# Optimization experiments

Hardware: AMD Instinct MI355X
Metric: run time of the kernel (lower is better)

## Reference

```python
import jax, jax.numpy as jnp
import numpy as np

N_NODES = 100000
N_EDGES = 1600000
N_GRAPHS = 64
DIMS = [128, 128, 128, 128]
IN_CH = 4


def setup_inputs() -> dict:
    key = jax.random.key(0)
    ks = jax.random.split(key, 24)
    d = {}
    d['x'] = jax.random.normal(ks[0], (N_NODES, IN_CH), dtype=jnp.float32)
    d['metadata'] = jax.random.normal(ks[1], (N_GRAPHS, 1), dtype=jnp.float32)
    d['edge_index'] = jax.random.randint(ks[2], (2, N_EDGES), 0, N_NODES, dtype=jnp.int32)
    d['batch'] = jnp.sort(jax.random.randint(ks[3], (N_NODES,), 0, N_GRAPHS, dtype=jnp.int32))
    dims_in = [IN_CH] + DIMS[:-1]
    ki = 4
    for i, (din, dout) in enumerate(zip(dims_in, DIMS), start=1):
        s = 1.0 / np.sqrt(din)
        d[f'w_rel{i}'] = jax.random.normal(ks[ki], (din, dout), dtype=jnp.float32) * s; ki += 1
        d[f'b_rel{i}'] = jnp.zeros((dout,), dtype=jnp.float32)
        d[f'w_root{i}'] = jax.random.normal(ks[ki], (din, dout), dtype=jnp.float32) * s; ki += 1
    d['convm_w'] = jax.random.normal(ks[ki], (4,), dtype=jnp.float32); ki += 1
    d['convm_b'] = jnp.zeros((4,), dtype=jnp.float32)
    fin = DIMS[3] * 2 + 4
    d['fc_w'] = jax.random.normal(ks[ki], (fin, DIMS[3]), dtype=jnp.float32) / np.sqrt(fin); ki += 1
    d['fc_b'] = jnp.zeros((DIMS[3],), dtype=jnp.float32)
    d['fc2_w'] = jax.random.normal(ks[ki], (DIMS[3], 1), dtype=jnp.float32) / np.sqrt(DIMS[3]); ki += 1
    d['fc2_b'] = jnp.zeros((1,), dtype=jnp.float32)
    return d


def _graph_conv(x, src, dst, w_rel, b_rel, w_root):
    # PyG GraphConv (aggr='add'): out_i = lin_rel(sum_{j->i} x_j) + lin_root(x_i)
    agg = jax.ops.segment_sum(x[src], dst, num_segments=N_NODES)
    return agg @ w_rel + b_rel + x @ w_root


def reference(x, metadata, edge_index, batch,
              w_rel1, b_rel1, w_root1,
              w_rel2, b_rel2, w_root2,
              w_rel3, b_rel3, w_root3,
              w_rel4, b_rel4, w_root4,
              convm_w, convm_b, fc_w, fc_b, fc2_w, fc2_b):
    src, dst = edge_index[0], edge_index[1]
    h = jax.nn.relu(_graph_conv(x, src, dst, w_rel1, b_rel1, w_root1))
    h = jax.nn.relu(_graph_conv(h, src, dst, w_rel2, b_rel2, w_root2))
    h = jax.nn.relu(_graph_conv(h, src, dst, w_rel3, b_rel3, w_root3))
    h = jax.nn.relu(_graph_conv(h, src, dst, w_rel4, b_rel4, w_root4))
    # global pools per graph
    counts = jax.ops.segment_sum(jnp.ones((N_NODES,), h.dtype), batch, num_segments=N_GRAPHS)
    x_sum = jax.ops.segment_sum(h, batch, num_segments=N_GRAPHS)
    x_mean = x_sum / jnp.maximum(counts, 1.0)[:, None]
    x_max = jax.ops.segment_max(h, batch, num_segments=N_GRAPHS)
    x_max = jnp.where(counts[:, None] > 0, x_max, 0.0)
    # metadata branch: Conv1d(1,4,k=1) on [B,1,1] -> [B,4]
    m = jax.nn.relu(metadata * convm_w[None, :] + convm_b[None, :])  # [B,4]
    x_c = jnp.concatenate([x_max, x_mean, m], axis=1)  # [B, 2*d+4]
    out = jax.nn.relu(x_c @ fc_w + fc_b) @ fc2_w + fc2_b
    return out[:, 0]
```

## Files before the change

kernel.cpp:

```cpp
#include <hip/hip_runtime.h>

#define N_NODES 100000
#define N_EDGES 1600000
#define N_GRAPHS 64

typedef __attribute__((ext_vector_type(8))) short bf16x8;
typedef __attribute__((ext_vector_type(4))) float f32x4;

__device__ __forceinline__ unsigned int f2bf(float f) {
  unsigned int u = __float_as_uint(f);
  return (u + 0x7FFFu + ((u >> 16) & 1u)) >> 16;
}
#define BLO(u) __uint_as_float((u) << 16)
#define BHI(u) __uint_as_float((u) & 0xFFFF0000u)

__device__ __forceinline__ void split8(const float* __restrict__ p, bf16x8& hi, bf16x8& lo) {
  float4 v0 = *(const float4*)p;
  float4 v1 = *(const float4*)(p + 4);
  unsigned h0 = f2bf(v0.x), h1 = f2bf(v0.y), h2 = f2bf(v0.z), h3 = f2bf(v0.w);
  unsigned h4 = f2bf(v1.x), h5 = f2bf(v1.y), h6 = f2bf(v1.z), h7 = f2bf(v1.w);
  hi[0] = (short)h0; hi[1] = (short)h1; hi[2] = (short)h2; hi[3] = (short)h3;
  hi[4] = (short)h4; hi[5] = (short)h5; hi[6] = (short)h6; hi[7] = (short)h7;
  lo[0] = (short)f2bf(v0.x - __uint_as_float(h0 << 16));
  lo[1] = (short)f2bf(v0.y - __uint_as_float(h1 << 16));
  lo[2] = (short)f2bf(v0.z - __uint_as_float(h2 << 16));
  lo[3] = (short)f2bf(v0.w - __uint_as_float(h3 << 16));
  lo[4] = (short)f2bf(v1.x - __uint_as_float(h4 << 16));
  lo[5] = (short)f2bf(v1.y - __uint_as_float(h5 << 16));
  lo[6] = (short)f2bf(v1.z - __uint_as_float(h6 << 16));
  lo[7] = (short)f2bf(v1.w - __uint_as_float(h7 << 16));
}


__global__ __launch_bounds__(256) void k_zero_int(int* __restrict__ p, int n) {
  int i = blockIdx.x * 256 + threadIdx.x;
  if (i < n) p[i] = 0;
}

__global__ __launch_bounds__(256) void k_hist(const int* __restrict__ ei, int* __restrict__ deg) {
  int e = blockIdx.x * 256 + threadIdx.x;
  if (e < N_EDGES) atomicAdd(&deg[ei[N_EDGES + e]], 1);
}

__global__ __launch_bounds__(256) void k_scan1(const int* __restrict__ deg, int* __restrict__ part,
                                               int* __restrict__ bsum) {
  __shared__ int tmp[256];
  int i = blockIdx.x * 256 + threadIdx.x;
  int v = (i < N_NODES) ? deg[i] : 0;
  tmp[threadIdx.x] = v;
  __syncthreads();
  for (int o = 1; o < 256; o <<= 1) {
    int t = (threadIdx.x >= o) ? tmp[threadIdx.x - o] : 0;
    __syncthreads();
    tmp[threadIdx.x] += t;
    __syncthreads();
  }
  if (i < N_NODES) part[i] = tmp[threadIdx.x] - v;
  if (threadIdx.x == 255) bsum[blockIdx.x] = tmp[255];
}

__global__ __launch_bounds__(512) void k_scan2(const int* __restrict__ bsum, int* __restrict__ boff, int nb) {
  __shared__ int tmp[512];
  int v = ((int)threadIdx.x < nb) ? bsum[threadIdx.x] : 0;
  tmp[threadIdx.x] = v;
  __syncthreads();
  for (int o = 1; o < 512; o <<= 1) {
    int t = (threadIdx.x >= o) ? tmp[threadIdx.x - o] : 0;
    __syncthreads();
    tmp[threadIdx.x] += t;
    __syncthreads();
  }
  if ((int)threadIdx.x < nb) boff[threadIdx.x] = tmp[threadIdx.x] - v;
}

__global__ __launch_bounds__(256) void k_scan3(const int* __restrict__ part, const int* __restrict__ boff,
                                               int* __restrict__ rowptr, int* __restrict__ cursor) {
  int i = blockIdx.x * 256 + threadIdx.x;
  if (i < N_NODES) {
    int r = part[i] + boff[i >> 8];
    rowptr[i] = r;
    cursor[i] = r;
  } else if (i == N_NODES) {
    rowptr[N_NODES] = N_EDGES;
  }
}

#define FW_NPW 12500
#define FW_EPS 12500
__global__ __launch_bounds__(256) void k_fill_win(const int* __restrict__ ei, int* __restrict__ cursor,
                                                  int* __restrict__ csr) {
  int bid = blockIdx.x;
  int w = bid & 7;
  int s = bid >> 3;
  int lo = w * FW_NPW, hi = lo + FW_NPW;
  int e0 = s * FW_EPS, e1 = e0 + FW_EPS;
  for (int e = e0 + threadIdx.x; e < e1; e += 256) {
    int d = ei[N_EDGES + e];
    if (d >= lo && d < hi) {
      int p = atomicAdd(&cursor[d], 1);
      csr[p] = ei[e];
    }
  }
}

__global__ __launch_bounds__(256) void k_prep_w(const float* __restrict__ w, unsigned short* __restrict__ wt) {
  int t = blockIdx.x * 256 + threadIdx.x;
  int k = t >> 7, c = t & 127;
  float v = w[k * 128 + c];
  unsigned int hi = f2bf(v);
  float vhi = __uint_as_float(hi << 16);
  unsigned int lo = f2bf(v - vhi);
  wt[c * 256 + k] = (unsigned short)hi;
  wt[c * 256 + k + 128] = (unsigned short)lo;
}


__global__ __launch_bounds__(256) void k_l1_agg(const float* __restrict__ x, const int* __restrict__ rowptr,
                                                const int* __restrict__ csr, float* __restrict__ agg4) {
  int t = blockIdx.x * 256 + threadIdx.x;
  if (t >= N_NODES * 4) return;
  int node = t >> 2, c = t & 3;
  int s = rowptr[node], e = rowptr[node + 1];
  float a = 0.f;
  for (int p = s; p < e; ++p) a += x[(size_t)csr[p] * 4 + c];
  agg4[t] = a;
}

__global__ __launch_bounds__(256) void k_l1_comb(const float* __restrict__ x, const float* __restrict__ agg4,
                                                 const float* __restrict__ w_rel, const float* __restrict__ b_rel,
                                                 const float* __restrict__ w_root, float* __restrict__ out,
                                                 unsigned short* __restrict__ hb) {
  int t = blockIdx.x * 256 + threadIdx.x;
  int node = t >> 7, c = t & 127;
  if (node >= N_NODES) return;
  float acc = b_rel[c];
#pragma unroll
  for (int k = 0; k < 4; ++k) acc += agg4[node * 4 + k] * w_rel[k * 128 + c];
#pragma unroll
  for (int k = 0; k < 4; ++k) acc += x[node * 4 + k] * w_root[k * 128 + c];
  float r = fmaxf(acc, 0.f);
  out[(size_t)node * 128 + c] = r;
  hb[(size_t)node * 128 + c] = (unsigned short)f2bf(r);
}

#define AGG_ACC(U)                                                    \
  a0.x += BLO((U).x); a0.y += BHI((U).x);                             \
  a0.z += BLO((U).y); a0.w += BHI((U).y);                             \
  a1.x += BLO((U).z); a1.y += BHI((U).z);                             \
  a1.z += BLO((U).w); a1.w += BHI((U).w);

__global__ __launch_bounds__(256) void k_agg_bf(const unsigned short* __restrict__ hb,
                                                const int* __restrict__ rowptr, const int* __restrict__ csr,
                                                float* __restrict__ aggout) {
  int node = (blockIdx.x * 256 + threadIdx.x) >> 4;
  int l = threadIdx.x & 15;
  if (node >= N_NODES) return;
  int s = rowptr[node], e = rowptr[node + 1];
  float4 a0 = make_float4(0.f, 0.f, 0.f, 0.f);
  float4 a1 = make_float4(0.f, 0.f, 0.f, 0.f);
  int p = s;
  for (; p + 4 <= e; p += 4) {
    int s0 = csr[p], s1 = csr[p + 1], s2 = csr[p + 2], s3 = csr[p + 3];
    uint4 u0 = *(const uint4*)&hb[(size_t)s0 * 128 + l * 8];
    uint4 u1 = *(const uint4*)&hb[(size_t)s1 * 128 + l * 8];
    uint4 u2 = *(const uint4*)&hb[(size_t)s2 * 128 + l * 8];
    uint4 u3 = *(const uint4*)&hb[(size_t)s3 * 128 + l * 8];
    AGG_ACC(u0)
    AGG_ACC(u1)
    AGG_ACC(u2)
    AGG_ACC(u3)
  }
  for (; p < e; ++p) {
    int s0 = csr[p];
    uint4 u = *(const uint4*)&hb[(size_t)s0 * 128 + l * 8];
    AGG_ACC(u)
  }
  *(float4*)&aggout[(size_t)node * 128 + l * 8] = a0;
  *(float4*)&aggout[(size_t)node * 128 + l * 8 + 4] = a1;
}

__global__ __launch_bounds__(256) void k_gemm_mfma3(
    const float* __restrict__ agg, const float* __restrict__ h,
    const unsigned short* __restrict__ wrelT, const unsigned short* __restrict__ wrootT,
    const float* __restrict__ bias, const int last,
    float* __restrict__ hout, unsigned short* __restrict__ hbout) {
  __shared__ char lds[32768];
  const int tid = threadIdx.x;
  const int wave = tid >> 6;
  const int lane = tid & 63;
  const int l15 = lane & 15;
  const int lg = lane >> 4;
  const int rb = blockIdx.x * 64 + wave * 16;
  int ar = rb + l15;
  if (ar >= N_NODES) ar = N_NODES - 1;

  f32x4 acc[8];
#pragma unroll
  for (int i = 0; i < 8; ++i) acc[i] = (f32x4){0.f, 0.f, 0.f, 0.f};

#pragma unroll
  for (int src = 0; src < 2; ++src) {
    const float* A = src ? h : agg;
    const unsigned short* W = src ? wrootT : wrelT;
    const float* arow = A + (size_t)ar * 128 + lg * 8;
    bf16x8 ah0, al0, ah1, al1, ah2, al2, ah3, al3;
    split8(arow, ah0, al0);
    split8(arow + 32, ah1, al1);
    split8(arow + 64, ah2, al2);
    split8(arow + 96, ah3, al3);
#pragma unroll
    for (int half = 0; half < 2; ++half) {
      __syncthreads();
      const unsigned short* wsrc = W + half * 16384;
#pragma unroll
      for (int i = 0; i < 8; ++i) {
        int f = i * 2048 + tid * 8;
        int col = f >> 8;
        int kb2 = (f & 255) * 2;
        uint4 v = *(const uint4*)(wsrc + f);
        *(uint4*)&lds[col * 512 + (kb2 ^ ((col & 7) << 4))] = v;
      }
      __syncthreads();
#pragma unroll
      for (int c0l = 0; c0l < 4; ++c0l) {
        const int c0 = half * 4 + c0l;
        const int cl = c0l * 16 + l15;
        const char* bp = lds + cl * 512;
        const int sw = (cl & 7) << 4;
        const int o = lg * 16;
        bf16x8 bh0 = *(const bf16x8*)(bp + ((o) ^ sw));
        bf16x8 bh1 = *(const bf16x8*)(bp + ((64 + o) ^ sw));
        bf16x8 bh2 = *(const bf16x8*)(bp + ((128 + o) ^ sw));
        bf16x8 bh3 = *(const bf16x8*)(bp + ((192 + o) ^ sw));
        bf16x8 bl0 = *(const bf16x8*)(bp + ((256 + o) ^ sw));
        bf16x8 bl1 = *(const bf16x8*)(bp + ((320 + o) ^ sw));
        bf16x8 bl2 = *(const bf16x8*)(bp + ((384 + o) ^ sw));
        bf16x8 bl3 = *(const bf16x8*)(bp + ((448 + o) ^ sw));
        acc[c0] = __builtin_amdgcn_mfma_f32_16x16x32_bf16(ah0, bh0, acc[c0], 0, 0, 0);
        acc[c0] = __builtin_amdgcn_mfma_f32_16x16x32_bf16(ah1, bh1, acc[c0], 0, 0, 0);
        acc[c0] = __builtin_amdgcn_mfma_f32_16x16x32_bf16(ah2, bh2, acc[c0], 0, 0, 0);
        acc[c0] = __builtin_amdgcn_mfma_f32_16x16x32_bf16(ah3, bh3, acc[c0], 0, 0, 0);
        acc[c0] = __builtin_amdgcn_mfma_f32_16x16x32_bf16(ah0, bl0, acc[c0], 0, 0, 0);
        acc[c0] = __builtin_amdgcn_mfma_f32_16x16x32_bf16(ah1, bl1, acc[c0], 0, 0, 0);
        acc[c0] = __builtin_amdgcn_mfma_f32_16x16x32_bf16(ah2, bl2, acc[c0], 0, 0, 0);
        acc[c0] = __builtin_amdgcn_mfma_f32_16x16x32_bf16(ah3, bl3, acc[c0], 0, 0, 0);
        acc[c0] = __builtin_amdgcn_mfma_f32_16x16x32_bf16(al0, bh0, acc[c0], 0, 0, 0);
        acc[c0] = __builtin_amdgcn_mfma_f32_16x16x32_bf16(al1, bh1, acc[c0], 0, 0, 0);
        acc[c0] = __builtin_amdgcn_mfma_f32_16x16x32_bf16(al2, bh2, acc[c0], 0, 0, 0);
        acc[c0] = __builtin_amdgcn_mfma_f32_16x16x32_bf16(al3, bh3, acc[c0], 0, 0, 0);
      }
    }
  }

#pragma unroll
  for (int c0 = 0; c0 < 8; ++c0) {
    const int c = c0 * 16 + l15;
    const float bi = bias[c];
#pragma unroll
    for (int j = 0; j < 4; ++j) {
      const int row = rb + lg * 4 + j;
      if (row < N_NODES) {
        float v = fmaxf(acc[c0][j] + bi, 0.f);
        hout[(size_t)row * 128 + c] = v;
        if (!last) hbout[(size_t)row * 128 + c] = (unsigned short)f2bf(v);
      }
    }
  }
}


__device__ __forceinline__ int lower_bound_batch(const int* __restrict__ batch, int key) {
  int lo = 0, hi = N_NODES;
  while (lo < hi) {
    int mid = (lo + hi) >> 1;
    if (batch[mid] < key) lo = mid + 1;
    else hi = mid;
  }
  return lo;
}

__global__ __launch_bounds__(256) void k_pool1(const float* __restrict__ h, const int* __restrict__ batch,
                                               float* __restrict__ psum, float* __restrict__ pmax) {
  int b = blockIdx.x;
  int g = b >> 2, q = b & 3;
  int start = lower_bound_batch(batch, g);
  int end = lower_bound_batch(batch, g + 1);
  int c = threadIdx.x & 127;
  int half = threadIdx.x >> 7;
  float sum = 0.f, mx = -3.0e38f;
  for (int n = start + q * 2 + half; n < end; n += 8) {
    float v = h[(size_t)n * 128 + c];
    sum += v;
    mx = fmaxf(mx, v);
  }
  __shared__ float ss[128], sm[128];
  if (half == 0) { ss[c] = sum; sm[c] = mx; }
  __syncthreads();
  if (half == 1) { ss[c] += sum; sm[c] = fmaxf(sm[c], mx); }
  __syncthreads();
  if (half == 0) {
    psum[(size_t)b * 128 + c] = ss[c];
    pmax[(size_t)b * 128 + c] = sm[c];
  }
}

__global__ __launch_bounds__(128) void k_pool2(const float* __restrict__ psum, const float* __restrict__ pmax,
                                               const int* __restrict__ batch, float* __restrict__ pooled) {
  int g = blockIdx.x;
  int c = threadIdx.x;
  int start = lower_bound_batch(batch, g), end = lower_bound_batch(batch, g + 1);
  int count = end - start;
  float s = 0.f, m = -3.0e38f;
#pragma unroll
  for (int q = 0; q < 4; ++q) {
    s += psum[(size_t)(g * 4 + q) * 128 + c];
    m = fmaxf(m, pmax[(size_t)(g * 4 + q) * 128 + c]);
  }
  pooled[(size_t)g * 256 + c] = (count > 0) ? m : 0.f;
  pooled[(size_t)g * 256 + 128 + c] = s / fmaxf((float)count, 1.f);
}


__global__ __launch_bounds__(128) void k_fc(const float* __restrict__ pooled, const float* __restrict__ metadata,
                                            const float* __restrict__ convm_w, const float* __restrict__ convm_b,
                                            const float* __restrict__ fc_w, const float* __restrict__ fc_b,
                                            const float* __restrict__ fc2_w, const float* __restrict__ fc2_b,
                                            float* __restrict__ out) {
  int g = blockIdx.x;
  int tid = threadIdx.x;
  __shared__ float xc[260];
  xc[tid] = pooled[(size_t)g * 256 + tid];
  xc[128 + tid] = pooled[(size_t)g * 256 + 128 + tid];
  if (tid < 4) xc[256 + tid] = fmaxf(metadata[g] * convm_w[tid] + convm_b[tid], 0.f);
  __syncthreads();
  float acc = fc_b[tid];
  for (int k = 0; k < 260; ++k) acc += xc[k] * fc_w[(size_t)k * 128 + tid];
  float partial = fmaxf(acc, 0.f) * fc2_w[tid];
#pragma unroll
  for (int off = 32; off > 0; off >>= 1) partial += __shfl_down(partial, off);
  __shared__ float wred[2];
  if ((tid & 63) == 0) wred[tid >> 6] = partial;
  __syncthreads();
  if (tid == 0) out[g] = wred[0] + wred[1] + fc2_b[0];
}


extern "C" void kernel_launch(void* const* d_in, const int* in_sizes, int n_in,
                              void* d_out, int out_size, void* d_ws, size_t ws_size,
                              hipStream_t stream) {
  const float* x = (const float*)d_in[0];
  const float* metadata = (const float*)d_in[1];
  const int* ei = (const int*)d_in[2];
  const int* batch = (const int*)d_in[3];
  const float* w_rel[4] = {(const float*)d_in[4], (const float*)d_in[7], (const float*)d_in[10], (const float*)d_in[13]};
  const float* b_rel[4] = {(const float*)d_in[5], (const float*)d_in[8], (const float*)d_in[11], (const float*)d_in[14]};
  const float* w_root[4] = {(const float*)d_in[6], (const float*)d_in[9], (const float*)d_in[12], (const float*)d_in[15]};
  const float* convm_w = (const float*)d_in[16];
  const float* convm_b = (const float*)d_in[17];
  const float* fc_w = (const float*)d_in[18];
  const float* fc_b = (const float*)d_in[19];
  const float* fc2_w = (const float*)d_in[20];
  const float* fc2_b = (const float*)d_in[21];
  float* out = (float*)d_out;

  char* ws = (char*)d_ws;
  size_t off = 0;
  auto alloc = [&](size_t bytes) {
    off = (off + 255) & ~(size_t)255;
    void* p = ws + off;
    off += bytes;
    return p;
  };
  int* deg = (int*)alloc((size_t)N_NODES * 4);
  int* rowptr = (int*)alloc((size_t)(N_NODES + 1) * 4);
  int* cursor = (int*)alloc((size_t)N_NODES * 4);
  int* bsum = (int*)alloc(512 * 4);
  int* boff = (int*)alloc(512 * 4);
  int* csr = (int*)alloc((size_t)N_EDGES * 4);
  float* agg4 = (float*)alloc((size_t)N_NODES * 4 * 4);
  float* bufA = (float*)alloc((size_t)N_NODES * 128 * 4);
  float* bufB = (float*)alloc((size_t)N_NODES * 128 * 4);
  unsigned short* hb = (unsigned short*)alloc((size_t)N_NODES * 128 * 2);
  unsigned short* wt = (unsigned short*)alloc((size_t)6 * 128 * 256 * 2);
  float* psum = (float*)alloc((size_t)256 * 128 * 4);
  float* pmax = (float*)alloc((size_t)256 * 128 * 4);
  float* pooled = (float*)alloc((size_t)64 * 256 * 4);

  const int nblk_nodes = (N_NODES + 255) / 256;
  const int nblk_edges = (N_EDGES + 255) / 256;

  for (int l = 1; l < 4; ++l) {
    k_prep_w<<<64, 256, 0, stream>>>(w_rel[l], wt + (size_t)(2 * (l - 1)) * 32768);
    k_prep_w<<<64, 256, 0, stream>>>(w_root[l], wt + (size_t)(2 * (l - 1) + 1) * 32768);
  }

  k_zero_int<<<nblk_nodes, 256, 0, stream>>>(deg, N_NODES);
  k_hist<<<nblk_edges, 256, 0, stream>>>(ei, deg);
  k_scan1<<<nblk_nodes, 256, 0, stream>>>(deg, rowptr, bsum);
  k_scan2<<<1, 512, 0, stream>>>(bsum, boff, nblk_nodes);
  k_scan3<<<(N_NODES + 1 + 255) / 256, 256, 0, stream>>>(rowptr, boff, rowptr, cursor);
  k_fill_win<<<8 * 128, 256, 0, stream>>>(ei, cursor, csr);

  k_l1_agg<<<(N_NODES * 4 + 255) / 256, 256, 0, stream>>>(x, rowptr, csr, agg4);
  k_l1_comb<<<(N_NODES * 128 + 255) / 256, 256, 0, stream>>>(x, agg4, w_rel[0], b_rel[0], w_root[0], bufA, hb);

  for (int l = 1; l < 4; ++l) {
    k_agg_bf<<<(N_NODES * 16 + 255) / 256, 256, 0, stream>>>(hb, rowptr, csr, bufB);
    k_gemm_mfma3<<<(N_NODES + 63) / 64, 256, 0, stream>>>(
        bufB, bufA, wt + (size_t)(2 * (l - 1)) * 32768, wt + (size_t)(2 * (l - 1) + 1) * 32768,
        b_rel[l], (l == 3) ? 1 : 0, bufA, hb);
  }

  k_pool1<<<256, 256, 0, stream>>>(bufA, batch, psum, pmax);
  k_pool2<<<64, 128, 0, stream>>>(psum, pmax, batch, pooled);
  k_fc<<<64, 128, 0, stream>>>(pooled, metadata, convm_w, convm_b, fc_w, fc_b, fc2_w, fc2_b, out);
}
```

Measured before the change: 733.7 us.

## Fuse neighbor aggregation into the MFMA GEMM kernel via LDS staging

```diff
diff --git a/kernel.cpp b/kernel.cpp
--- a/kernel.cpp
+++ b/kernel.cpp
@@ -14,9 +14,7 @@
 #define BLO(u) __uint_as_float((u) << 16)
 #define BHI(u) __uint_as_float((u) & 0xFFFF0000u)
 
-__device__ __forceinline__ void split8(const float* __restrict__ p, bf16x8& hi, bf16x8& lo) {
-  float4 v0 = *(const float4*)p;
-  float4 v1 = *(const float4*)(p + 4);
+__device__ __forceinline__ void split8v(float4 v0, float4 v1, bf16x8& hi, bf16x8& lo) {
   unsigned h0 = f2bf(v0.x), h1 = f2bf(v0.y), h2 = f2bf(v0.z), h3 = f2bf(v0.w);
   unsigned h4 = f2bf(v1.x), h5 = f2bf(v1.y), h6 = f2bf(v1.z), h7 = f2bf(v1.w);
   hi[0] = (short)h0; hi[1] = (short)h1; hi[2] = (short)h2; hi[3] = (short)h3;
@@ -29,6 +27,10 @@
   lo[5] = (short)f2bf(v1.y - __uint_as_float(h5 << 16));
   lo[6] = (short)f2bf(v1.z - __uint_as_float(h6 << 16));
   lo[7] = (short)f2bf(v1.w - __uint_as_float(h7 << 16));
+}
+
+__device__ __forceinline__ void split8(const float* __restrict__ p, bf16x8& hi, bf16x8& lo) {
+  split8v(*(const float4*)p, *(const float4*)(p + 4), hi, lo);
 }
 
 
@@ -149,38 +151,9 @@
   a1.x += BLO((U).z); a1.y += BHI((U).z);                             \
   a1.z += BLO((U).w); a1.w += BHI((U).w);
 
-__global__ __launch_bounds__(256) void k_agg_bf(const unsigned short* __restrict__ hb,
-                                                const int* __restrict__ rowptr, const int* __restrict__ csr,
-                                                float* __restrict__ aggout) {
-  int node = (blockIdx.x * 256 + threadIdx.x) >> 4;
-  int l = threadIdx.x & 15;
-  if (node >= N_NODES) return;
-  int s = rowptr[node], e = rowptr[node + 1];
-  float4 a0 = make_float4(0.f, 0.f, 0.f, 0.f);
-  float4 a1 = make_float4(0.f, 0.f, 0.f, 0.f);
-  int p = s;
-  for (; p + 4 <= e; p += 4) {
-    int s0 = csr[p], s1 = csr[p + 1], s2 = csr[p + 2], s3 = csr[p + 3];
-    uint4 u0 = *(const uint4*)&hb[(size_t)s0 * 128 + l * 8];
-    uint4 u1 = *(const uint4*)&hb[(size_t)s1 * 128 + l * 8];
-    uint4 u2 = *(const uint4*)&hb[(size_t)s2 * 128 + l * 8];
-    uint4 u3 = *(const uint4*)&hb[(size_t)s3 * 128 + l * 8];
-    AGG_ACC(u0)
-    AGG_ACC(u1)
-    AGG_ACC(u2)
-    AGG_ACC(u3)
-  }
-  for (; p < e; ++p) {
-    int s0 = csr[p];
-    uint4 u = *(const uint4*)&hb[(size_t)s0 * 128 + l * 8];
-    AGG_ACC(u)
-  }
-  *(float4*)&aggout[(size_t)node * 128 + l * 8] = a0;
-  *(float4*)&aggout[(size_t)node * 128 + l * 8 + 4] = a1;
-}
-
-__global__ __launch_bounds__(256) void k_gemm_mfma3(
-    const float* __restrict__ agg, const float* __restrict__ h,
+__global__ __launch_bounds__(256) void k_agg_gemm(
+    const unsigned short* __restrict__ hbin, const float* __restrict__ h,
+    const int* __restrict__ rowptr, const int* __restrict__ csr,
     const unsigned short* __restrict__ wrelT, const unsigned short* __restrict__ wrootT,
     const float* __restrict__ bias, const int last,
     float* __restrict__ hout, unsigned short* __restrict__ hbout) {
@@ -191,23 +164,93 @@
   const int l15 = lane & 15;
   const int lg = lane >> 4;
   const int rb = blockIdx.x * 64 + wave * 16;
+
+  {
+    const int gl = tid & 15;
+    for (int it = 0; it < 4; ++it) {
+      int nl = it * 16 + (tid >> 4);
+      int node = blockIdx.x * 64 + nl;
+      if (node >= N_NODES) node = N_NODES - 1;
+      int s = rowptr[node], e = rowptr[node + 1];
+      float4 a0 = make_float4(0.f, 0.f, 0.f, 0.f);
+      float4 a1 = make_float4(0.f, 0.f, 0.f, 0.f);
+      int p = s;
+      for (; p + 8 <= e; p += 8) {
+        int s0 = csr[p], s1 = csr[p + 1], s2 = csr[p + 2], s3 = csr[p + 3];
+        int s4 = csr[p + 4], s5 = csr[p + 5], s6 = csr[p + 6], s7 = csr[p + 7];
+        uint4 u0 = *(const uint4*)&hbin[(size_t)s0 * 128 + gl * 8];
+        uint4 u1 = *(const uint4*)&hbin[(size_t)s1 * 128 + gl * 8];
+        uint4 u2 = *(const uint4*)&hbin[(size_t)s2 * 128 + gl * 8];
+        uint4 u3 = *(const uint4*)&hbin[(size_t)s3 * 128 + gl * 8];
+        uint4 u4 = *(const uint4*)&hbin[(size_t)s4 * 128 + gl * 8];
+        uint4 u5 = *(const uint4*)&hbin[(size_t)s5 * 128 + gl * 8];
+        uint4 u6 = *(const uint4*)&hbin[(size_t)s6 * 128 + gl * 8];
+        uint4 u7 = *(const uint4*)&hbin[(size_t)s7 * 128 + gl * 8];
+        AGG_ACC(u0) AGG_ACC(u1) AGG_ACC(u2) AGG_ACC(u3)
+        AGG_ACC(u4) AGG_ACC(u5) AGG_ACC(u6) AGG_ACC(u7)
+      }
+      for (; p + 4 <= e; p += 4) {
+        int s0 = csr[p], s1 = csr[p + 1], s2 = csr[p + 2], s3 = csr[p + 3];
+        uint4 u0 = *(const uint4*)&hbin[(size_t)s0 * 128 + gl * 8];
+        uint4 u1 = *(const uint4*)&hbin[(size_t)s1 * 128 + gl * 8];
+        uint4 u2 = *(const uint4*)&hbin[(size_t)s2 * 128 + gl * 8];
+        uint4 u3 = *(const uint4*)&hbin[(size_t)s3 * 128 + gl * 8];
+        AGG_ACC(u0) AGG_ACC(u1) AGG_ACC(u2) AGG_ACC(u3)
+      }
+      for (; p < e; ++p) {
+        int s0 = csr[p];
+        uint4 u = *(const uint4*)&hbin[(size_t)s0 * 128 + gl * 8];
+        AGG_ACC(u)
+      }
+      int sw = (nl & 7) << 4;
+      *(float4*)&lds[nl * 512 + ((gl * 32) ^ sw)] = a0;
+      *(float4*)&lds[nl * 512 + ((gl * 32 + 16) ^ sw)] = a1;
+    }
+  }
+  __syncthreads();
+
+  bf16x8 rh0, rl0, rh1, rl1, rh2, rl2, rh3, rl3;
+  {
+    const int row = wave * 16 + l15;
+    const int sw = (row & 7) << 4;
+    const char* bp = lds + row * 512;
+    const int o = lg * 32;
+    float4 v0, v1;
+    v0 = *(const float4*)(bp + ((o) ^ sw));
+    v1 = *(const float4*)(bp + ((o + 16) ^ sw));
+    split8v(v0, v1, rh0, rl0);
+    v0 = *(const float4*)(bp + ((128 + o) ^ sw));
+    v1 = *(const float4*)(bp + ((128 + o + 16) ^ sw));
+    split8v(v0, v1, rh1, rl1);
+    v0 = *(const float4*)(bp + ((256 + o) ^ sw));
+    v1 = *(const float4*)(bp + ((256 + o + 16) ^ sw));
+    split8v(v0, v1, rh2, rl2);
+    v0 = *(const float4*)(bp + ((384 + o) ^ sw));
+    v1 = *(const float4*)(bp + ((384 + o + 16) ^ sw));
+    split8v(v0, v1, rh3, rl3);
+  }
+
+  f32x4 acc[8];
+#pragma unroll
+  for (int i = 0; i < 8; ++i) acc[i] = (f32x4){0.f, 0.f, 0.f, 0.f};
+
   int ar = rb + l15;
   if (ar >= N_NODES) ar = N_NODES - 1;
 
-  f32x4 acc[8];
-#pragma unroll
-  for (int i = 0; i < 8; ++i) acc[i] = (f32x4){0.f, 0.f, 0.f, 0.f};
-
 #pragma unroll
   for (int src = 0; src < 2; ++src) {
-    const float* A = src ? h : agg;
     const unsigned short* W = src ? wrootT : wrelT;
-    const float* arow = A + (size_t)ar * 128 + lg * 8;
     bf16x8 ah0, al0, ah1, al1, ah2, al2, ah3, al3;
-    split8(arow, ah0, al0);
-    split8(arow + 32, ah1, al1);
-    split8(arow + 64, ah2, al2);
-    split8(arow + 96, ah3, al3);
+    if (src == 0) {
+      ah0 = rh0; al0 = rl0; ah1 = rh1; al1 = rl1;
+      ah2 = rh2; al2 = rl2; ah3 = rh3; al3 = rl3;
+    } else {
+      const float* arow = h + (size_t)ar * 128 + lg * 8;
+      split8(arow, ah0, al0);
+      split8(arow + 32, ah1, al1);
+      split8(arow + 64, ah2, al2);
+      split8(arow + 96, ah3, al3);
+    }
 #pragma unroll
     for (int half = 0; half < 2; ++half) {
       __syncthreads();
@@ -379,8 +422,8 @@
   int* csr = (int*)alloc((size_t)N_EDGES * 4);
   float* agg4 = (float*)alloc((size_t)N_NODES * 4 * 4);
   float* bufA = (float*)alloc((size_t)N_NODES * 128 * 4);
-  float* bufB = (float*)alloc((size_t)N_NODES * 128 * 4);
-  unsigned short* hb = (unsigned short*)alloc((size_t)N_NODES * 128 * 2);
+  unsigned short* hb1 = (unsigned short*)alloc((size_t)N_NODES * 128 * 2);
+  unsigned short* hb2 = (unsigned short*)alloc((size_t)N_NODES * 128 * 2);
   unsigned short* wt = (unsigned short*)alloc((size_t)6 * 128 * 256 * 2);
   float* psum = (float*)alloc((size_t)256 * 128 * 4);
   float* pmax = (float*)alloc((size_t)256 * 128 * 4);
@@ -402,13 +445,15 @@
   k_fill_win<<<8 * 128, 256, 0, stream>>>(ei, cursor, csr);
 
   k_l1_agg<<<(N_NODES * 4 + 255) / 256, 256, 0, stream>>>(x, rowptr, csr, agg4);
-  k_l1_comb<<<(N_NODES * 128 + 255) / 256, 256, 0, stream>>>(x, agg4, w_rel[0], b_rel[0], w_root[0], bufA, hb);
+  k_l1_comb<<<(N_NODES * 128 + 255) / 256, 256, 0, stream>>>(x, agg4, w_rel[0], b_rel[0], w_root[0], bufA, hb1);
 
   for (int l = 1; l < 4; ++l) {
-    k_agg_bf<<<(N_NODES * 16 + 255) / 256, 256, 0, stream>>>(hb, rowptr, csr, bufB);
-    k_gemm_mfma3<<<(N_NODES + 63) / 64, 256, 0, stream>>>(
-        bufB, bufA, wt + (size_t)(2 * (l - 1)) * 32768, wt + (size_t)(2 * (l - 1) + 1) * 32768,
-        b_rel[l], (l == 3) ? 1 : 0, bufA, hb);
+    const unsigned short* hsrc = (l & 1) ? hb1 : hb2;
+    unsigned short* hdst = (l & 1) ? hb2 : hb1;
+    k_agg_gemm<<<(N_NODES + 63) / 64, 256, 0, stream>>>(
+        hsrc, bufA, rowptr, csr,
+        wt + (size_t)(2 * (l - 1)) * 32768, wt + (size_t)(2 * (l - 1) + 1) * 32768,
+        b_rel[l], (l == 3) ? 1 : 0, bufA, hdst);
   }
 
   k_pool1<<<256, 256, 0, stream>>>(bufA, batch, psum, pmax);
```

Result: slower. 764.1 us (+4.1%).

## Store activations and aggregates as split bf16 hi/lo planes instead of fp32

Applied to the files above, without the earlier changes.

```diff
diff --git a/kernel.cpp b/kernel.cpp
--- a/kernel.cpp
+++ b/kernel.cpp
@@ -14,21 +14,17 @@
 #define BLO(u) __uint_as_float((u) << 16)
 #define BHI(u) __uint_as_float((u) & 0xFFFF0000u)
 
-__device__ __forceinline__ void split8(const float* __restrict__ p, bf16x8& hi, bf16x8& lo) {
-  float4 v0 = *(const float4*)p;
-  float4 v1 = *(const float4*)(p + 4);
-  unsigned h0 = f2bf(v0.x), h1 = f2bf(v0.y), h2 = f2bf(v0.z), h3 = f2bf(v0.w);
-  unsigned h4 = f2bf(v1.x), h5 = f2bf(v1.y), h6 = f2bf(v1.z), h7 = f2bf(v1.w);
-  hi[0] = (short)h0; hi[1] = (short)h1; hi[2] = (short)h2; hi[3] = (short)h3;
-  hi[4] = (short)h4; hi[5] = (short)h5; hi[6] = (short)h6; hi[7] = (short)h7;
-  lo[0] = (short)f2bf(v0.x - __uint_as_float(h0 << 16));
-  lo[1] = (short)f2bf(v0.y - __uint_as_float(h1 << 16));
-  lo[2] = (short)f2bf(v0.z - __uint_as_float(h2 << 16));
-  lo[3] = (short)f2bf(v0.w - __uint_as_float(h3 << 16));
-  lo[4] = (short)f2bf(v1.x - __uint_as_float(h4 << 16));
-  lo[5] = (short)f2bf(v1.y - __uint_as_float(h5 << 16));
-  lo[6] = (short)f2bf(v1.z - __uint_as_float(h6 << 16));
-  lo[7] = (short)f2bf(v1.w - __uint_as_float(h7 << 16));
+__device__ __forceinline__ void pack_hilo8(const float* v, uint4& hi, uint4& lo) {
+  unsigned hb_[8], lb_[8];
+#pragma unroll
+  for (int i = 0; i < 8; ++i) {
+    hb_[i] = f2bf(v[i]);
+    lb_[i] = f2bf(v[i] - __uint_as_float(hb_[i] << 16));
+  }
+  hi.x = hb_[0] | (hb_[1] << 16); hi.y = hb_[2] | (hb_[3] << 16);
+  hi.z = hb_[4] | (hb_[5] << 16); hi.w = hb_[6] | (hb_[7] << 16);
+  lo.x = lb_[0] | (lb_[1] << 16); lo.y = lb_[2] | (lb_[3] << 16);
+  lo.z = lb_[4] | (lb_[5] << 16); lo.w = lb_[6] | (lb_[7] << 16);
 }
 
 
@@ -128,8 +124,8 @@
 
 __global__ __launch_bounds__(256) void k_l1_comb(const float* __restrict__ x, const float* __restrict__ agg4,
                                                  const float* __restrict__ w_rel, const float* __restrict__ b_rel,
-                                                 const float* __restrict__ w_root, float* __restrict__ out,
-                                                 unsigned short* __restrict__ hb) {
+                                                 const float* __restrict__ w_root,
+                                                 unsigned short* __restrict__ hh, unsigned short* __restrict__ hl) {
   int t = blockIdx.x * 256 + threadIdx.x;
   int node = t >> 7, c = t & 127;
   if (node >= N_NODES) return;
@@ -139,8 +135,9 @@
 #pragma unroll
   for (int k = 0; k < 4; ++k) acc += x[node * 4 + k] * w_root[k * 128 + c];
   float r = fmaxf(acc, 0.f);
-  out[(size_t)node * 128 + c] = r;
-  hb[(size_t)node * 128 + c] = (unsigned short)f2bf(r);
+  unsigned int hb_ = f2bf(r);
+  hh[(size_t)node * 128 + c] = (unsigned short)hb_;
+  hl[(size_t)node * 128 + c] = (unsigned short)f2bf(r - __uint_as_float(hb_ << 16));
 }
 
 #define AGG_ACC(U)                                                    \
@@ -149,9 +146,10 @@
   a1.x += BLO((U).z); a1.y += BHI((U).z);                             \
   a1.z += BLO((U).w); a1.w += BHI((U).w);
 
-__global__ __launch_bounds__(256) void k_agg_bf(const unsigned short* __restrict__ hb,
+__global__ __launch_bounds__(256) void k_agg_bf(const unsigned short* __restrict__ hh,
                                                 const int* __restrict__ rowptr, const int* __restrict__ csr,
-                                                float* __restrict__ aggout) {
+                                                unsigned short* __restrict__ aggh,
+                                                unsigned short* __restrict__ aggl) {
   int node = (blockIdx.x * 256 + threadIdx.x) >> 4;
   int l = threadIdx.x & 15;
   if (node >= N_NODES) return;
@@ -159,31 +157,47 @@
   float4 a0 = make_float4(0.f, 0.f, 0.f, 0.f);
   float4 a1 = make_float4(0.f, 0.f, 0.f, 0.f);
   int p = s;
+  for (; p + 8 <= e; p += 8) {
+    int s0 = csr[p], s1 = csr[p + 1], s2 = csr[p + 2], s3 = csr[p + 3];
+    int s4 = csr[p + 4], s5 = csr[p + 5], s6 = csr[p + 6], s7 = csr[p + 7];
+    uint4 u0 = *(const uint4*)&hh[(size_t)s0 * 128 + l * 8];
+    uint4 u1 = *(const uint4*)&hh[(size_t)s1 * 128 + l * 8];
+    uint4 u2 = *(const uint4*)&hh[(size_t)s2 * 128 + l * 8];
+    uint4 u3 = *(const uint4*)&hh[(size_t)s3 * 128 + l * 8];
+    uint4 u4 = *(const uint4*)&hh[(size_t)s4 * 128 + l * 8];
+    uint4 u5 = *(const uint4*)&hh[(size_t)s5 * 128 + l * 8];
+    uint4 u6 = *(const uint4*)&hh[(size_t)s6 * 128 + l * 8];
+    uint4 u7 = *(const uint4*)&hh[(size_t)s7 * 128 + l * 8];
+    AGG_ACC(u0) AGG_ACC(u1) AGG_ACC(u2) AGG_ACC(u3)
+    AGG_ACC(u4) AGG_ACC(u5) AGG_ACC(u6) AGG_ACC(u7)
+  }
   for (; p + 4 <= e; p += 4) {
     int s0 = csr[p], s1 = csr[p + 1], s2 = csr[p + 2], s3 = csr[p + 3];
-    uint4 u0 = *(const uint4*)&hb[(size_t)s0 * 128 + l * 8];
-    uint4 u1 = *(const uint4*)&hb[(size_t)s1 * 128 + l * 8];
-    uint4 u2 = *(const uint4*)&hb[(size_t)s2 * 128 + l * 8];
-    uint4 u3 = *(const uint4*)&hb[(size_t)s3 * 128 + l * 8];
-    AGG_ACC(u0)
-    AGG_ACC(u1)
-    AGG_ACC(u2)
-    AGG_ACC(u3)
+    uint4 u0 = *(const uint4*)&hh[(size_t)s0 * 128 + l * 8];
+    uint4 u1 = *(const uint4*)&hh[(size_t)s1 * 128 + l * 8];
+    uint4 u2 = *(const uint4*)&hh[(size_t)s2 * 128 + l * 8];
+    uint4 u3 = *(const uint4*)&hh[(size_t)s3 * 128 + l * 8];
+    AGG_ACC(u0) AGG_ACC(u1) AGG_ACC(u2) AGG_ACC(u3)
   }
   for (; p < e; ++p) {
     int s0 = csr[p];
-    uint4 u = *(const uint4*)&hb[(size_t)s0 * 128 + l * 8];
+    uint4 u = *(const uint4*)&hh[(size_t)s0 * 128 + l * 8];
     AGG_ACC(u)
   }
-  *(float4*)&aggout[(size_t)node * 128 + l * 8] = a0;
-  *(float4*)&aggout[(size_t)node * 128 + l * 8 + 4] = a1;
-}
-
-__global__ __launch_bounds__(256) void k_gemm_mfma3(
-    const float* __restrict__ agg, const float* __restrict__ h,
+  float v[8] = {a0.x, a0.y, a0.z, a0.w, a1.x, a1.y, a1.z, a1.w};
+  uint4 hi, lo;
+  pack_hilo8(v, hi, lo);
+  *(uint4*)&aggh[(size_t)node * 128 + l * 8] = hi;
+  *(uint4*)&aggl[(size_t)node * 128 + l * 8] = lo;
+}
+
+__global__ __launch_bounds__(256) void k_gemm_mfma4(
+    const unsigned short* __restrict__ aggh, const unsigned short* __restrict__ aggl,
+    const unsigned short* __restrict__ hh, const unsigned short* __restrict__ hl,
     const unsigned short* __restrict__ wrelT, const unsigned short* __restrict__ wrootT,
     const float* __restrict__ bias, const int last,
-    float* __restrict__ hout, unsigned short* __restrict__ hbout) {
+    float* __restrict__ fout,
+    unsigned short* __restrict__ hho, unsigned short* __restrict__ hlo) {
   __shared__ char lds[32768];
   const int tid = threadIdx.x;
   const int wave = tid >> 6;
@@ -200,14 +214,18 @@
 
 #pragma unroll
   for (int src = 0; src < 2; ++src) {
-    const float* A = src ? h : agg;
+    const unsigned short* Ah = src ? hh : aggh;
+    const unsigned short* Al = src ? hl : aggl;
     const unsigned short* W = src ? wrootT : wrelT;
-    const float* arow = A + (size_t)ar * 128 + lg * 8;
-    bf16x8 ah0, al0, ah1, al1, ah2, al2, ah3, al3;
-    split8(arow, ah0, al0);
-    split8(arow + 32, ah1, al1);
-    split8(arow + 64, ah2, al2);
-    split8(arow + 96, ah3, al3);
+    const size_t abase = (size_t)ar * 128 + lg * 8;
+    bf16x8 ah0 = *(const bf16x8*)&Ah[abase];
+    bf16x8 ah1 = *(const bf16x8*)&Ah[abase + 32];
+    bf16x8 ah2 = *(const bf16x8*)&Ah[abase + 64];
+    bf16x8 ah3 = *(const bf16x8*)&Ah[abase + 96];
+    bf16x8 al0 = *(const bf16x8*)&Al[abase];
+    bf16x8 al1 = *(const bf16x8*)&Al[abase + 32];
+    bf16x8 al2 = *(const bf16x8*)&Al[abase + 64];
+    bf16x8 al3 = *(const bf16x8*)&Al[abase + 96];
 #pragma unroll
     for (int half = 0; half < 2; ++half) {
       __syncthreads();
@@ -261,8 +279,13 @@
       const int row = rb + lg * 4 + j;
       if (row < N_NODES) {
         float v = fmaxf(acc[c0][j] + bi, 0.f);
-        hout[(size_t)row * 128 + c] = v;
-        if (!last) hbout[(size_t)row * 128 + c] = (unsigned short)f2bf(v);
+        if (last) {
+          fout[(size_t)row * 128 + c] = v;
+        } else {
+          unsigned int hb_ = f2bf(v);
+          hho[(size_t)row * 128 + c] = (unsigned short)hb_;
+          hlo[(size_t)row * 128 + c] = (unsigned short)f2bf(v - __uint_as_float(hb_ << 16));
+        }
       }
     }
   }
@@ -379,8 +402,10 @@
   int* csr = (int*)alloc((size_t)N_EDGES * 4);
   float* agg4 = (float*)alloc((size_t)N_NODES * 4 * 4);
   float* bufA = (float*)alloc((size_t)N_NODES * 128 * 4);
-  float* bufB = (float*)alloc((size_t)N_NODES * 128 * 4);
-  unsigned short* hb = (unsigned short*)alloc((size_t)N_NODES * 128 * 2);
+  unsigned short* hh = (unsigned short*)alloc((size_t)N_NODES * 128 * 2);
+  unsigned short* hl = (unsigned short*)alloc((size_t)N_NODES * 128 * 2);
+  unsigned short* aggh = (unsigned short*)alloc((size_t)N_NODES * 128 * 2);
+  unsigned short* aggl = (unsigned short*)alloc((size_t)N_NODES * 128 * 2);
   unsigned short* wt = (unsigned short*)alloc((size_t)6 * 128 * 256 * 2);
   float* psum = (float*)alloc((size_t)256 * 128 * 4);
   float* pmax = (float*)alloc((size_t)256 * 128 * 4);
@@ -402,13 +427,14 @@
   k_fill_win<<<8 * 128, 256, 0, stream>>>(ei, cursor, csr);
 
   k_l1_agg<<<(N_NODES * 4 + 255) / 256, 256, 0, stream>>>(x, rowptr, csr, agg4);
-  k_l1_comb<<<(N_NODES * 128 + 255) / 256, 256, 0, stream>>>(x, agg4, w_rel[0], b_rel[0], w_root[0], bufA, hb);
+  k_l1_comb<<<(N_NODES * 128 + 255) / 256, 256, 0, stream>>>(x, agg4, w_rel[0], b_rel[0], w_root[0], hh, hl);
 
   for (int l = 1; l < 4; ++l) {
-    k_agg_bf<<<(N_NODES * 16 + 255) / 256, 256, 0, stream>>>(hb, rowptr, csr, bufB);
-    k_gemm_mfma3<<<(N_NODES + 63) / 64, 256, 0, stream>>>(
-        bufB, bufA, wt + (size_t)(2 * (l - 1)) * 32768, wt + (size_t)(2 * (l - 1) + 1) * 32768,
-        b_rel[l], (l == 3) ? 1 : 0, bufA, hb);
+    k_agg_bf<<<(N_NODES * 16 + 255) / 256, 256, 0, stream>>>(hh, rowptr, csr, aggh, aggl);
+    k_gemm_mfma4<<<(N_NODES + 63) / 64, 256, 0, stream>>>(
+        aggh, aggl, hh, hl,
+        wt + (size_t)(2 * (l - 1)) * 32768, wt + (size_t)(2 * (l - 1) + 1) * 32768,
+        b_rel[l], (l == 3) ? 1 : 0, bufA, hh, hl);
   }
 
   k_pool1<<<256, 256, 0, stream>>>(bufA, batch, psum, pmax);
```

After: 710.9 us. -3.1%, faster.
